# Kernel optimization log

Measured on AMD Instinct MI355X. Metric: run time of the kernel, lower is better.

The kernel has to match this reference:

```python
import jax, jax.numpy as jnp
import numpy as np

N_HEADS = 16
LN_EPS = 1e-5

def _layernorm(x, g, b):
    m = jnp.mean(x, axis=-1, keepdims=True)
    v = jnp.var(x, axis=-1, keepdims=True)
    return (x - m) * jax.lax.rsqrt(v + LN_EPS) * g + b

def setup_inputs() -> dict:
    key = jax.random.key(0)
    ks = jax.random.split(key, 6)
    B, L, D = 4, 1024, 1024
    Dff = 4 * D
    s = 0.02  # init scale to keep logits/activations in a sane range
    return {
        "X": jax.random.normal(ks[0], (B, L, D), jnp.float32),
        "wq": jax.random.normal(ks[1], (D, D), jnp.float32) * s,
        "wk": jax.random.normal(ks[2], (D, D), jnp.float32) * s,
        "wv": jax.random.normal(ks[3], (D, D), jnp.float32) * s,
        "ln1_g": jnp.ones((D,), jnp.float32),
        "ln1_b": jnp.zeros((D,), jnp.float32),
        "w1": jax.random.normal(ks[4], (Dff, D), jnp.float32) * s,
        "b1": jnp.zeros((Dff,), jnp.float32),
        "w2": jax.random.normal(ks[5], (D, Dff), jnp.float32) * s,
        "b2": jnp.zeros((D,), jnp.float32),
        "ln2_g": jnp.ones((D,), jnp.float32),
        "ln2_b": jnp.zeros((D,), jnp.float32),
    }

def reference(X, wq, wk, wv, ln1_g, ln1_b, w1, b1, w2, b2, ln2_g, ln2_b):
    B, L, D = X.shape
    H = N_HEADS
    dh = D // H
    # qkv projections (torch Linear: x @ W^T), split into heads
    Q = (X @ wq.T).reshape(B, L, H, dh)
    K = (X @ wk.T).reshape(B, L, H, dh)
    V = (X @ wv.T).reshape(B, L, H, dh)
    scores = jnp.einsum("blhd,bmhd->bhlm", Q, K)  # [B,H,L,L]
    causal = jnp.tril(jnp.ones((L, L), dtype=bool))
    scores = jnp.where(causal, scores, -jnp.inf)
    attn = jax.nn.softmax(scores / jnp.sqrt(jnp.asarray(dh, X.dtype)), axis=-1)
    ctx = jnp.einsum("bhlm,bmhd->blhd", attn, V).reshape(B, L, D)
    # post-LN residual (note: no output projection after attention)
    X = _layernorm(X + ctx, ln1_g, ln1_b)
    h = jax.nn.selu(X @ w1.T + b1)
    X = _layernorm(X + h @ w2.T + b2, ln2_g, ln2_b)
    return X
```

## Files before the change

kernel.cpp:

```cpp
#include <hip/hip_runtime.h>
#include <hip/hip_bf16.h>

#define BATCH 4
#define SEQ   1024
#define DIM   1024
#define NH    16
#define DH    64
#define DFF   4096
#define MTOK  (BATCH*SEQ)

#define QSCALE 0.1803368801111204f

typedef __attribute__((ext_vector_type(8))) short  short8;
typedef __attribute__((ext_vector_type(4))) short  short4v;
typedef __attribute__((ext_vector_type(4))) float  floatx4;
typedef __attribute__((ext_vector_type(4))) float  float4v;
typedef __attribute__((ext_vector_type(4))) int    int4v;

__device__ inline float bf2f(short s) {
    return __uint_as_float(((unsigned int)(unsigned short)s) << 16);
}
__device__ inline short f2bf(float f) {
    __hip_bfloat16 h = __float2bfloat16(f);
    return *reinterpret_cast<short*>(&h);
}

__device__ inline float wave_sum(float v) {
    #pragma unroll
    for (int off = 32; off >= 1; off >>= 1) v += __shfl_xor(v, off);
    return v;
}

__device__ inline void async_ld16(short* lds, const short* g) {
    __builtin_amdgcn_global_load_lds(
        (const __attribute__((address_space(1))) void*)g,
        (__attribute__((address_space(3))) void*)lds, 16, 0, 0);
}

#define GBAR() do { asm volatile("" ::: "memory");            \
                    __builtin_amdgcn_s_barrier();             \
                    asm volatile("" ::: "memory"); } while (0)

__global__ __launch_bounds__(256) void convert_all(
    const float* __restrict__ sX,  short* __restrict__ dX,
    const float* __restrict__ sq,  short* __restrict__ dq,
    const float* __restrict__ sk,  short* __restrict__ dk,
    const float* __restrict__ sv,  short* __restrict__ dv,
    const float* __restrict__ s1,  short* __restrict__ d1,
    const float* __restrict__ s2,  short* __restrict__ d2)
{
    int cid = blockIdx.x * 256 + threadIdx.x;
    const float* src; short* dst; int base;
    if      (cid <  524288) { src = sX; dst = dX; base = 0; }
    else if (cid <  655360) { src = sq; dst = dq; base = 524288; }
    else if (cid <  786432) { src = sk; dst = dk; base = 655360; }
    else if (cid <  917504) { src = sv; dst = dv; base = 786432; }
    else if (cid < 1441792) { src = s1; dst = d1; base = 917504; }
    else                    { src = s2; dst = d2; base = 1441792; }
    size_t i = (size_t)(cid - base) * 8;
    float4v f0 = *(const float4v*)(src + i);
    float4v f1 = *(const float4v*)(src + i + 4);
    short8 o;
    o[0]=f2bf(f0[0]); o[1]=f2bf(f0[1]); o[2]=f2bf(f0[2]); o[3]=f2bf(f0[3]);
    o[4]=f2bf(f1[0]); o[5]=f2bf(f1[1]); o[6]=f2bf(f1[2]); o[7]=f2bf(f1[3]);
    *(short8*)(dst + i) = o;
}

template<int EPI>
__global__ __launch_bounds__(512, 2) void gemm256(
    const short* __restrict__ A, const short* __restrict__ B,
    const float* __restrict__ bias, short* __restrict__ C, int N, int K)
{
    __shared__ __align__(16) short Ls[65536];

    const int t    = threadIdx.x;
    const int lane = t & 63;
    const int wave = t >> 6;
    const int quad = lane >> 4;
    const int l15  = lane & 15;
    const int wm   = wave >> 2;
    const int wn   = wave & 3;
    const int tm   = blockIdx.x * 256;
    const int tn   = blockIdx.y * 256;

    int kbase = 0, klen = K;
    if (EPI == 3) { klen = K >> 2; kbase = blockIdx.z * klen; }
    const int NT = klen >> 6;

    const int r0 = t >> 3;
    const int rb = ((t >> 8) & 1) * 64 + ((t >> 3) & 31);
    const int g8 = (((t & 7) ^ ((t >> 3) & 7)) << 3);
    const int offAL[2] = { r0*K + g8,          (128 + r0)*K + g8 };
    const int offAH[2] = { (64 + r0)*K + g8,   (192 + r0)*K + g8 };
    const int offB0[2] = { rb*K + g8,          (128 + rb)*K + g8 };
    const int offB1[2] = { (32 + rb)*K + g8,   (160 + rb)*K + g8 };
    const short* Abase = A + (size_t)tm * K + kbase;
    const short* Bbase = B + (size_t)tn * K + kbase;
    short* dstb = &Ls[t * 8];

    const int xa  = (wm*64 + l15) * 64;
    const int xb  = (wn*32 + l15) * 64;
    const int sw  = l15 & 7;
    const int xc0 = ((quad ^ sw) << 3);
    const int xc1 = (((4 + quad) ^ sw) << 3);

    short8 a[4][2], b[4][2];
    floatx4 acc[8][4];
    #pragma unroll
    for (int mt = 0; mt < 8; mt++)
        #pragma unroll
        for (int nt = 0; nt < 4; nt++) acc[mt][nt] = {0.f, 0.f, 0.f, 0.f};

#define STAGE(buf, slot, offs, base, k0) do {                         \
        short* _d = dstb + (buf)*32768 + (slot)*8192;                 \
        async_ld16(_d,        (base) + (offs)[0] + (k0));             \
        async_ld16(_d + 4096, (base) + (offs)[1] + (k0));             \
    } while (0)

#define LDA4(buf, hf) do { _Pragma("unroll")                          \
    for (int _mt = 0; _mt < 4; _mt++) {                               \
        a[_mt][0] = *(const short8*)&Ls[(buf)*32768 + (hf)*8192 + xa + _mt*1024 + xc0]; \
        a[_mt][1] = *(const short8*)&Ls[(buf)*32768 + (hf)*8192 + xa + _mt*1024 + xc1]; \
    } } while (0)

#define LDB4(buf) do { _Pragma("unroll")                              \
    for (int _bh = 0; _bh < 2; _bh++) { _Pragma("unroll")             \
        for (int _nn = 0; _nn < 2; _nn++) {                           \
            b[_bh*2+_nn][0] = *(const short8*)&Ls[(buf)*32768 + 16384 + _bh*8192 + xb + _nn*1024 + xc0]; \
            b[_bh*2+_nn][1] = *(const short8*)&Ls[(buf)*32768 + 16384 + _bh*8192 + xb + _nn*1024 + xc1]; \
        } } } while (0)

#define MM32(mb) do { __builtin_amdgcn_s_setprio(1); _Pragma("unroll") \
    for (int _c = 0; _c < 2; _c++) { _Pragma("unroll")                \
        for (int _mt = 0; _mt < 4; _mt++) { _Pragma("unroll")         \
            for (int _nn = 0; _nn < 4; _nn++) {                       \
                acc[(mb)+_mt][_nn] = __builtin_amdgcn_mfma_f32_16x16x32_bf16( \
                    a[_mt][_c], b[_nn][_c], acc[(mb)+_mt][_nn], 0, 0, 0);     \
            } } }                                                     \
    __builtin_amdgcn_s_setprio(0); } while (0)

    STAGE(0, 0, offAL, Abase, 0);
    STAGE(0, 2, offB0, Bbase, 0);
    STAGE(0, 3, offB1, Bbase, 0);
    STAGE(0, 1, offAH, Abase, 0);
    STAGE(1, 0, offAL, Abase, 64);
    STAGE(1, 2, offB0, Bbase, 64);
    STAGE(1, 3, offB1, Bbase, 64);
    asm volatile("s_waitcnt vmcnt(8)" ::: "memory");
    GBAR();

    for (int kt = 0; kt < NT; ++kt) {
        const int cur = (kt & 1), nxt = cur ^ 1;
        LDA4(cur, 0);
        LDB4(cur);
        if (kt + 1 < NT) STAGE(nxt, 1, offAH, Abase, (kt + 1) << 6);
        asm volatile("s_waitcnt lgkmcnt(0)" ::: "memory");
        if (kt < NT - 1) asm volatile("s_waitcnt vmcnt(8)" ::: "memory");
        else             asm volatile("s_waitcnt vmcnt(0)" ::: "memory");
        GBAR();
        MM32(0);
        LDA4(cur, 1);
        if (kt + 2 < NT) {
            STAGE(cur, 0, offAL, Abase, (kt + 2) << 6);
            STAGE(cur, 2, offB0, Bbase, (kt + 2) << 6);
            STAGE(cur, 3, offB1, Bbase, (kt + 2) << 6);
        }
        asm volatile("s_waitcnt lgkmcnt(0)" ::: "memory");
        if (kt < NT - 2)       asm volatile("s_waitcnt vmcnt(8)" ::: "memory");
        else if (kt == NT - 2) asm volatile("s_waitcnt vmcnt(2)" ::: "memory");
        else                   asm volatile("s_waitcnt vmcnt(0)" ::: "memory");
        GBAR();
        MM32(4);
    }

    const float SS = 1.0507009873554805f;
    const float SA = 1.6732632423543772f;

    #pragma unroll
    for (int mt = 0; mt < 8; mt++) {
        int row0 = tm + wm*128 + (mt >> 2)*64 + (mt & 3)*16 + quad*4;
        #pragma unroll
        for (int nt = 0; nt < 4; nt++) {
            int col = tn + wn*64 + nt*16 + l15;
            if (EPI == 0 && (col >> 10) == 2) {
                int h = (col >> 6) & 15, d = col & 63;
                int bb = row0 >> 10, key = row0 & 1023;
                short4v pv;
                #pragma unroll
                for (int r = 0; r < 4; r++) pv[r] = f2bf(acc[mt][nt][r]);
                *(short4v*)&C[(size_t)2*MTOK*1024
                    + ((size_t)(bb*16 + h)*64 + d)*1024 + key] = pv;
                continue;
            }
            #pragma unroll
            for (int r = 0; r < 4; r++) {
                int row = row0 + r;
                float v = acc[mt][nt][r];
                if (EPI == 0) {
                    int which = col >> 10;
                    if (which == 0) v *= QSCALE;
                    C[(size_t)which * ((size_t)MTOK*1024)
                      + (size_t)row * 1024 + (col & 1023)] = f2bf(v);
                } else if (EPI == 1) {
                    v += bias[col];
                    v = (v > 0.f) ? SS * v
                                  : SS * SA * (exp2f(v * 1.44269504f) - 1.f);
                    C[(size_t)row * N + col] = f2bf(v);
                } else {
                    C[(size_t)blockIdx.z * ((size_t)MTOK*N)
                      + (size_t)row * N + col] = f2bf(v);
                }
            }
        }
    }
#undef STAGE
#undef LDA4
#undef LDB4
#undef MM32
}

__global__ __launch_bounds__(256) void attn_kernel(
    const short* __restrict__ Q, const short* __restrict__ K,
    const short* __restrict__ Vt, short* __restrict__ CTX)
{
    __shared__ __align__(16) short Ks[2][64*64];
    __shared__ __align__(16) short Vs[2][64*64];
    __shared__ __align__(16) short Pl[4][32][72];

    const int t    = threadIdx.x;
    const int lane = t & 63;
    const int wave = t >> 6;
    const int quad = lane >> 4;
    const int l15  = lane & 15;
    const int q0 = (gridDim.x - 1 - blockIdx.x) * 128;
    const int bh = blockIdx.y;
    const int b  = bh >> 4;
    const int h  = bh & 15;

    const size_t headoff = (size_t)b * SEQ * DIM + (size_t)h * DH;
    const short* Qb  = Q + headoff;
    const short* Kb  = K + headoff;
    const short* Vtb = Vt + (size_t)bh * DH * SEQ;

    const int wrow0 = q0 + wave*32;

    short8 aq[2][2];
    #pragma unroll
    for (int mg = 0; mg < 2; mg++)
        #pragma unroll
        for (int c = 0; c < 2; c++)
            aq[mg][c] = *(const short8*)(Qb
                + (size_t)(wrow0 + mg*16 + l15) * DIM + c*32 + quad*8);

    short8 bones;
    {
        short v = (l15 == 0) ? (short)0x3F80 : (short)0;
        #pragma unroll
        for (int e = 0; e < 8; e++) bones[e] = v;
    }

    floatx4 o[2][4], ol[2];
    #pragma unroll
    for (int mg = 0; mg < 2; mg++) {
        #pragma unroll
        for (int nt = 0; nt < 4; nt++) o[mg][nt] = {0.f, 0.f, 0.f, 0.f};
        ol[mg] = {0.f, 0.f, 0.f, 0.f};
    }

    const int swz = (((t & 7) ^ ((t >> 3) & 7))) * 8;
    auto stage = [&](int j0, int sb) {
        #pragma unroll
        for (int p = 0; p < 2; p++) {
            async_ld16(Ks[sb] + (t + p*256)*8,
                       Kb + (size_t)(j0 + (t>>3) + p*32) * DIM + swz);
            async_ld16(Vs[sb] + (t + p*256)*8,
                       Vtb + (size_t)((t>>3) + p*32) * SEQ + j0 + swz);
        }
    };

    const int jend = q0 + 128;
    stage(0, 0);
    __syncthreads();

    int sb = 0;
    for (int j0 = 0; j0 < jend; j0 += 64) {
        if (j0 + 64 < jend) stage(j0 + 64, sb ^ 1);

        if (j0 <= wrow0 + 31) {
            floatx4 s[2][4];
            #pragma unroll
            for (int mg = 0; mg < 2; mg++)
                #pragma unroll
                for (int nt = 0; nt < 4; nt++) s[mg][nt] = {0.f, 0.f, 0.f, 0.f};
            #pragma unroll
            for (int c = 0; c < 2; c++) {
                #pragma unroll
                for (int nt = 0; nt < 4; nt++) {
                    short8 bk = *(const short8*)&Ks[sb][(nt*16 + l15)*64
                                  + ((c*4 + quad) ^ (l15 & 7))*8];
                    s[0][nt] = __builtin_amdgcn_mfma_f32_16x16x32_bf16(bk, aq[0][c], s[0][nt], 0, 0, 0);
                    s[1][nt] = __builtin_amdgcn_mfma_f32_16x16x32_bf16(bk, aq[1][c], s[1][nt], 0, 0, 0);
                }
            }

            if (j0 + 63 > wrow0) {
                #pragma unroll
                for (int mg = 0; mg < 2; mg++) {
                    int rowq = wrow0 + mg*16 + l15;
                    #pragma unroll
                    for (int nt = 0; nt < 4; nt++) {
                        #pragma unroll
                        for (int r = 0; r < 4; r++) {
                            int key = j0 + nt*16 + quad*4 + r;
                            if (key > rowq) s[mg][nt][r] = -1.0e38f;
                        }
                    }
                }
            }

            #pragma unroll
            for (int mg = 0; mg < 2; mg++)
                #pragma unroll
                for (int nt = 0; nt < 4; nt++) {
                    short4v pv;
                    #pragma unroll
                    for (int r = 0; r < 4; r++)
                        pv[r] = f2bf(exp2f(s[mg][nt][r]));
                    *(short4v*)&Pl[wave][mg*16 + l15][nt*16 + quad*4] = pv;
                }

            #pragma unroll
            for (int c = 0; c < 2; c++) {
                short8 ap0 = *(const short8*)&Pl[wave][l15][c*32 + quad*8];
                short8 ap1 = *(const short8*)&Pl[wave][16 + l15][c*32 + quad*8];
                #pragma unroll
                for (int nt = 0; nt < 4; nt++) {
                    short8 bv = *(const short8*)&Vs[sb][(nt*16 + l15)*64
                                  + ((c*4 + quad) ^ (l15 & 7))*8];
                    o[0][nt] = __builtin_amdgcn_mfma_f32_16x16x32_bf16(ap0, bv, o[0][nt], 0, 0, 0);
                    o[1][nt] = __builtin_amdgcn_mfma_f32_16x16x32_bf16(ap1, bv, o[1][nt], 0, 0, 0);
                }
                ol[0] = __builtin_amdgcn_mfma_f32_16x16x32_bf16(ap0, bones, ol[0], 0, 0, 0);
                ol[1] = __builtin_amdgcn_mfma_f32_16x16x32_bf16(ap1, bones, ol[1], 0, 0, 0);
            }
        }

        __syncthreads();
        sb ^= 1;
    }

    #pragma unroll
    for (int mg = 0; mg < 2; mg++) {
        float linv[4];
        #pragma unroll
        for (int r = 0; r < 4; r++)
            linv[r] = 1.f / __shfl(ol[mg][r], lane & 48);
        #pragma unroll
        for (int nt = 0; nt < 4; nt++) {
            #pragma unroll
            for (int r = 0; r < 4; r++) {
                int rowq = wrow0 + mg*16 + quad*4 + r;
                int d    = nt*16 + l15;
                CTX[(size_t)b * SEQ * DIM + (size_t)rowq * DIM + h*DH + d]
                    = f2bf(o[mg][nt][r] * linv[r]);
            }
        }
    }
}

__global__ __launch_bounds__(256) void ln1_kernel(
    const float* __restrict__ X, const short* __restrict__ ctx,
    const float* __restrict__ g, const float* __restrict__ bvec,
    short* __restrict__ out)
{
    __shared__ float red[8];
    const size_t base = (size_t)blockIdx.x * DIM;
    const int wave = threadIdx.x >> 6;

    float x[4];
    float sum = 0.f, sq = 0.f;
    #pragma unroll
    for (int i = 0; i < 4; i++) {
        int idx = threadIdx.x + i*256;
        float v = X[base + idx] + bf2f(ctx[base + idx]);
        x[i] = v; sum += v; sq += v*v;
    }
    sum = wave_sum(sum); sq = wave_sum(sq);
    if ((threadIdx.x & 63) == 0) { red[wave] = sum; red[4 + wave] = sq; }
    __syncthreads();
    float s1 = red[0] + red[1] + red[2] + red[3];
    float s2 = red[4] + red[5] + red[6] + red[7];
    float mean = s1 * (1.f / DIM);
    float var  = s2 * (1.f / DIM) - mean * mean;
    float rstd = rsqrtf(var + 1e-5f);
    #pragma unroll
    for (int i = 0; i < 4; i++) {
        int idx = threadIdx.x + i*256;
        out[base + idx] = f2bf((x[i] - mean) * rstd * g[idx] + bvec[idx]);
    }
}

__global__ __launch_bounds__(256) void ln2_fused(
    const short* __restrict__ P, const float* __restrict__ bias,
    const short* __restrict__ x1, const float* __restrict__ g,
    const float* __restrict__ bvec, float* __restrict__ out)
{
    __shared__ float red[8];
    const size_t base = (size_t)blockIdx.x * DIM;
    const size_t E4 = (size_t)MTOK * 1024;
    const int wave = threadIdx.x >> 6;

    float x[4];
    float sum = 0.f, sq = 0.f;
    #pragma unroll
    for (int i = 0; i < 4; i++) {
        int idx = threadIdx.x + i*256;
        size_t p = base + idx;
        float v = bf2f(P[p]) + bf2f(P[E4 + p]) + bf2f(P[2*E4 + p])
                + bf2f(P[3*E4 + p]) + bias[idx] + bf2f(x1[p]);
        x[i] = v; sum += v; sq += v*v;
    }
    sum = wave_sum(sum); sq = wave_sum(sq);
    if ((threadIdx.x & 63) == 0) { red[wave] = sum; red[4 + wave] = sq; }
    __syncthreads();
    float s1 = red[0] + red[1] + red[2] + red[3];
    float s2 = red[4] + red[5] + red[6] + red[7];
    float mean = s1 * (1.f / DIM);
    float var  = s2 * (1.f / DIM) - mean * mean;
    float rstd = rsqrtf(var + 1e-5f);
    #pragma unroll
    for (int i = 0; i < 4; i++) {
        int idx = threadIdx.x + i*256;
        out[base + idx] = (x[i] - mean) * rstd * g[idx] + bvec[idx];
    }
}

extern "C" void kernel_launch(void* const* d_in, const int* in_sizes, int n_in,
                              void* d_out, int out_size, void* d_ws, size_t ws_size,
                              hipStream_t stream)
{
    const float* X   = (const float*)d_in[0];
    const float* wq  = (const float*)d_in[1];
    const float* wk  = (const float*)d_in[2];
    const float* wv  = (const float*)d_in[3];
    const float* g1  = (const float*)d_in[4];
    const float* b1  = (const float*)d_in[5];
    const float* w1  = (const float*)d_in[6];
    const float* bb1 = (const float*)d_in[7];
    const float* w2  = (const float*)d_in[8];
    const float* bb2 = (const float*)d_in[9];
    const float* g2  = (const float*)d_in[10];
    const float* b2  = (const float*)d_in[11];

    short* ws = (short*)d_ws;
    const size_t E1 = 1048576, E4 = 4194304;
    size_t o = 0;
    short* Xb    = ws + o; o += E4;
    short* wqkvb = ws + o; o += 3*E1;
    short* w1b   = ws + o; o += E4;
    short* w2b   = ws + o; o += E4;
    short* Q     = ws + o; o += E4;
    short* Kb    = ws + o; o += E4;
    short* Vt    = ws + o; o += E4;
    short* CTX   = ws + o; o += E4;
    short* X1    = ws + o; o += E4;
    short* P     = ws + o; o += 4*E4;
    short* Hf    = Q;

    dim3 blk(256);
    convert_all<<<dim3(7680), blk, 0, stream>>>(
        X, Xb, wq, wqkvb, wk, wqkvb + E1, wv, wqkvb + 2*E1,
        w1, w1b, w2, w2b);

    gemm256<0><<<dim3(MTOK/256, 3072/256), dim3(512), 0, stream>>>(
        Xb, wqkvb, nullptr, Q, 3072, DIM);
    attn_kernel<<<dim3(SEQ/128, BATCH*NH), blk, 0, stream>>>(Q, Kb, Vt, CTX);
    ln1_kernel<<<dim3(MTOK), blk, 0, stream>>>(X, CTX, g1, b1, X1);
    gemm256<1><<<dim3(MTOK/256, DFF/256), dim3(512), 0, stream>>>(
        X1, w1b, bb1, Hf, DFF, DIM);
    gemm256<3><<<dim3(MTOK/256, DIM/256, 4), dim3(512), 0, stream>>>(
        Hf, w2b, nullptr, P, DIM, DFF);
    ln2_fused<<<dim3(MTOK), blk, 0, stream>>>(P, bb2, X1, g2, b2, (float*)d_out);
}
```

Measured before the change: 282.5 us.

## Replace 256x256 hand-pipelined GEMM with simpler 128x128 double-buffered GEMM

Replaces the 512-thread 256x256-tile GEMM, with its split-half staging and manual vmcnt waits, by a 256-thread 128x128-tile kernel. The new kernel double-buffers whole K-tiles and synchronises with plain __syncthreads. Smaller tiles give more blocks and less LDS per block, which may help occupancy and wave balance. In exchange each loaded element is reused less, and the finer load/compute interleaving of the old pipeline is lost.

Result: no change. 278.5 us (-1.4%).

```diff
diff --git a/kernel.cpp b/kernel.cpp
--- a/kernel.cpp
+++ b/kernel.cpp
@@ -36,10 +36,6 @@
         (const __attribute__((address_space(1))) void*)g,
         (__attribute__((address_space(3))) void*)lds, 16, 0, 0);
 }
-
-#define GBAR() do { asm volatile("" ::: "memory");            \
-                    __builtin_amdgcn_s_barrier();             \
-                    asm volatile("" ::: "memory"); } while (0)
 
 __global__ __launch_bounds__(256) void convert_all(
     const float* __restrict__ sX,  short* __restrict__ dX,
@@ -67,118 +63,87 @@
 }
 
 template<int EPI>
-__global__ __launch_bounds__(512, 2) void gemm256(
+__global__ __launch_bounds__(256, 2) void gemm128d(
     const short* __restrict__ A, const short* __restrict__ B,
     const float* __restrict__ bias, short* __restrict__ C, int N, int K)
 {
-    __shared__ __align__(16) short Ls[65536];
+    __shared__ __align__(16) short Ls[32768];
 
     const int t    = threadIdx.x;
     const int lane = t & 63;
     const int wave = t >> 6;
     const int quad = lane >> 4;
     const int l15  = lane & 15;
-    const int wm   = wave >> 2;
-    const int wn   = wave & 3;
-    const int tm   = blockIdx.x * 256;
-    const int tn   = blockIdx.y * 256;
+    const int wm   = wave & 1;
+    const int wn   = wave >> 1;
+    const int tm   = blockIdx.x * 128;
+    const int tn   = blockIdx.y * 128;
 
     int kbase = 0, klen = K;
     if (EPI == 3) { klen = K >> 2; kbase = blockIdx.z * klen; }
     const int NT = klen >> 6;
 
-    const int r0 = t >> 3;
-    const int rb = ((t >> 8) & 1) * 64 + ((t >> 3) & 31);
     const int g8 = (((t & 7) ^ ((t >> 3) & 7)) << 3);
-    const int offAL[2] = { r0*K + g8,          (128 + r0)*K + g8 };
-    const int offAH[2] = { (64 + r0)*K + g8,   (192 + r0)*K + g8 };
-    const int offB0[2] = { rb*K + g8,          (128 + rb)*K + g8 };
-    const int offB1[2] = { (32 + rb)*K + g8,   (160 + rb)*K + g8 };
+    int offR[4];
+    #pragma unroll
+    for (int i = 0; i < 4; i++) offR[i] = (i*32 + (t >> 3)) * K + g8;
     const short* Abase = A + (size_t)tm * K + kbase;
     const short* Bbase = B + (size_t)tn * K + kbase;
     short* dstb = &Ls[t * 8];
 
     const int xa  = (wm*64 + l15) * 64;
-    const int xb  = (wn*32 + l15) * 64;
+    const int xb  = (wn*64 + l15) * 64;
     const int sw  = l15 & 7;
     const int xc0 = ((quad ^ sw) << 3);
     const int xc1 = (((4 + quad) ^ sw) << 3);
 
     short8 a[4][2], b[4][2];
-    floatx4 acc[8][4];
-    #pragma unroll
-    for (int mt = 0; mt < 8; mt++)
+    floatx4 acc[4][4];
+    #pragma unroll
+    for (int mt = 0; mt < 4; mt++)
         #pragma unroll
         for (int nt = 0; nt < 4; nt++) acc[mt][nt] = {0.f, 0.f, 0.f, 0.f};
 
-#define STAGE(buf, slot, offs, base, k0) do {                         \
-        short* _d = dstb + (buf)*32768 + (slot)*8192;                 \
-        async_ld16(_d,        (base) + (offs)[0] + (k0));             \
-        async_ld16(_d + 4096, (base) + (offs)[1] + (k0));             \
-    } while (0)
-
-#define LDA4(buf, hf) do { _Pragma("unroll")                          \
+#define STAGE_TILE(buf, k0) do { _Pragma("unroll")                    \
+    for (int _i = 0; _i < 4; _i++) {                                  \
+        async_ld16(dstb + (buf)*16384 + _i*2048,        Abase + offR[_i] + (k0)); \
+        async_ld16(dstb + (buf)*16384 + 8192 + _i*2048, Bbase + offR[_i] + (k0)); \
+    } } while (0)
+
+#define LDAB(buf) do { _Pragma("unroll")                              \
     for (int _mt = 0; _mt < 4; _mt++) {                               \
-        a[_mt][0] = *(const short8*)&Ls[(buf)*32768 + (hf)*8192 + xa + _mt*1024 + xc0]; \
-        a[_mt][1] = *(const short8*)&Ls[(buf)*32768 + (hf)*8192 + xa + _mt*1024 + xc1]; \
+        a[_mt][0] = *(const short8*)&Ls[(buf)*16384 + xa + _mt*1024 + xc0]; \
+        a[_mt][1] = *(const short8*)&Ls[(buf)*16384 + xa + _mt*1024 + xc1]; \
+        b[_mt][0] = *(const short8*)&Ls[(buf)*16384 + 8192 + xb + _mt*1024 + xc0]; \
+        b[_mt][1] = *(const short8*)&Ls[(buf)*16384 + 8192 + xb + _mt*1024 + xc1]; \
     } } while (0)
 
-#define LDB4(buf) do { _Pragma("unroll")                              \
-    for (int _bh = 0; _bh < 2; _bh++) { _Pragma("unroll")             \
-        for (int _nn = 0; _nn < 2; _nn++) {                           \
-            b[_bh*2+_nn][0] = *(const short8*)&Ls[(buf)*32768 + 16384 + _bh*8192 + xb + _nn*1024 + xc0]; \
-            b[_bh*2+_nn][1] = *(const short8*)&Ls[(buf)*32768 + 16384 + _bh*8192 + xb + _nn*1024 + xc1]; \
-        } } } while (0)
-
-#define MM32(mb) do { __builtin_amdgcn_s_setprio(1); _Pragma("unroll") \
+#define MM32() do { __builtin_amdgcn_s_setprio(1); _Pragma("unroll")  \
     for (int _c = 0; _c < 2; _c++) { _Pragma("unroll")                \
         for (int _mt = 0; _mt < 4; _mt++) { _Pragma("unroll")         \
             for (int _nn = 0; _nn < 4; _nn++) {                       \
-                acc[(mb)+_mt][_nn] = __builtin_amdgcn_mfma_f32_16x16x32_bf16( \
-                    a[_mt][_c], b[_nn][_c], acc[(mb)+_mt][_nn], 0, 0, 0);     \
+                acc[_mt][_nn] = __builtin_amdgcn_mfma_f32_16x16x32_bf16( \
+                    a[_mt][_c], b[_nn][_c], acc[_mt][_nn], 0, 0, 0);  \
             } } }                                                     \
     __builtin_amdgcn_s_setprio(0); } while (0)
 
-    STAGE(0, 0, offAL, Abase, 0);
-    STAGE(0, 2, offB0, Bbase, 0);
-    STAGE(0, 3, offB1, Bbase, 0);
-    STAGE(0, 1, offAH, Abase, 0);
-    STAGE(1, 0, offAL, Abase, 64);
-    STAGE(1, 2, offB0, Bbase, 64);
-    STAGE(1, 3, offB1, Bbase, 64);
-    asm volatile("s_waitcnt vmcnt(8)" ::: "memory");
-    GBAR();
+    STAGE_TILE(0, 0);
+    __syncthreads();
 
     for (int kt = 0; kt < NT; ++kt) {
-        const int cur = (kt & 1), nxt = cur ^ 1;
-        LDA4(cur, 0);
-        LDB4(cur);
-        if (kt + 1 < NT) STAGE(nxt, 1, offAH, Abase, (kt + 1) << 6);
-        asm volatile("s_waitcnt lgkmcnt(0)" ::: "memory");
-        if (kt < NT - 1) asm volatile("s_waitcnt vmcnt(8)" ::: "memory");
-        else             asm volatile("s_waitcnt vmcnt(0)" ::: "memory");
-        GBAR();
-        MM32(0);
-        LDA4(cur, 1);
-        if (kt + 2 < NT) {
-            STAGE(cur, 0, offAL, Abase, (kt + 2) << 6);
-            STAGE(cur, 2, offB0, Bbase, (kt + 2) << 6);
-            STAGE(cur, 3, offB1, Bbase, (kt + 2) << 6);
-        }
-        asm volatile("s_waitcnt lgkmcnt(0)" ::: "memory");
-        if (kt < NT - 2)       asm volatile("s_waitcnt vmcnt(8)" ::: "memory");
-        else if (kt == NT - 2) asm volatile("s_waitcnt vmcnt(2)" ::: "memory");
-        else                   asm volatile("s_waitcnt vmcnt(0)" ::: "memory");
-        GBAR();
-        MM32(4);
+        const int cur = kt & 1;
+        if (kt + 1 < NT) STAGE_TILE(cur ^ 1, (kt + 1) << 6);
+        LDAB(cur);
+        MM32();
+        __syncthreads();
     }
 
     const float SS = 1.0507009873554805f;
     const float SA = 1.6732632423543772f;
 
     #pragma unroll
-    for (int mt = 0; mt < 8; mt++) {
-        int row0 = tm + wm*128 + (mt >> 2)*64 + (mt & 3)*16 + quad*4;
+    for (int mt = 0; mt < 4; mt++) {
+        int row0 = tm + wm*64 + mt*16 + quad*4;
         #pragma unroll
         for (int nt = 0; nt < 4; nt++) {
             int col = tn + wn*64 + nt*16 + l15;
@@ -213,9 +178,8 @@
             }
         }
     }
-#undef STAGE
-#undef LDA4
-#undef LDB4
+#undef STAGE_TILE
+#undef LDAB
 #undef MM32
 }
 
@@ -472,13 +436,13 @@
         X, Xb, wq, wqkvb, wk, wqkvb + E1, wv, wqkvb + 2*E1,
         w1, w1b, w2, w2b);
 
-    gemm256<0><<<dim3(MTOK/256, 3072/256), dim3(512), 0, stream>>>(
+    gemm128d<0><<<dim3(MTOK/128, 3072/128), blk, 0, stream>>>(
         Xb, wqkvb, nullptr, Q, 3072, DIM);
     attn_kernel<<<dim3(SEQ/128, BATCH*NH), blk, 0, stream>>>(Q, Kb, Vt, CTX);
     ln1_kernel<<<dim3(MTOK), blk, 0, stream>>>(X, CTX, g1, b1, X1);
-    gemm256<1><<<dim3(MTOK/256, DFF/256), dim3(512), 0, stream>>>(
+    gemm128d<1><<<dim3(MTOK/128, DFF/128), blk, 0, stream>>>(
         X1, w1b, bb1, Hf, DFF, DIM);
-    gemm256<3><<<dim3(MTOK/256, DIM/256, 4), dim3(512), 0, stream>>>(
+    gemm128d<3><<<dim3(MTOK/128, DIM/128, 4), blk, 0, stream>>>(
         Hf, w2b, nullptr, P, DIM, DFF);
     ln2_fused<<<dim3(MTOK), blk, 0, stream>>>(P, bb2, X1, g2, b2, (float*)d_out);
 }
```
